# Performance work log

Measured on AMD Instinct MI355X. Metric: run time of the kernel, lower is better.

## Reference

```python
import jax, jax.numpy as jnp
import numpy as np

NUM_GRAPHS = 512


def setup_inputs() -> dict:
    key = jax.random.key(0)
    ks = jax.random.split(key, 12)
    N, E, D, H, C = 100000, 1600000, 128, 128, 10
    x = jax.random.normal(ks[0], (N, D), dtype=jnp.float32)
    edge_index = jax.random.randint(ks[1], (2, E), 0, N, dtype=jnp.int64)
    batch = jnp.sort(jax.random.randint(ks[2], (N,), 0, NUM_GRAPHS, dtype=jnp.int64))
    def glorot(k, fan_in, fan_out):
        s = jnp.sqrt(6.0 / (fan_in + fan_out))
        return jax.random.uniform(k, (fan_in, fan_out), jnp.float32, -s, s)
    return {
        "x": x, "edge_index": edge_index, "batch": batch,
        "W_init": glorot(ks[3], D, H), "b_init": jnp.zeros((H,), jnp.float32),
        "W_h0": glorot(ks[4], H, H), "b_h0": jnp.zeros((H,), jnp.float32),
        "W_h1": glorot(ks[5], H, H), "b_h1": jnp.zeros((H,), jnp.float32),
        "W_out": glorot(ks[6], H, C), "b_out": jnp.zeros((C,), jnp.float32),
    }


def reference(x, edge_index, batch, W_init, b_init, W_h0, b_h0, W_h1, b_h1, W_out, b_out):
    N = x.shape[0]
    loop = jnp.arange(N, dtype=edge_index.dtype)
    # add self-loops (PyG GCNConv default)
    row = jnp.concatenate([edge_index[0], loop])  # source
    col = jnp.concatenate([edge_index[1], loop])  # target
    # symmetric normalization D^-1/2 (A+I) D^-1/2, degrees on target index
    deg = jax.ops.segment_sum(jnp.ones_like(col, dtype=x.dtype), col, num_segments=N)
    dis = jnp.where(deg > 0, jax.lax.rsqrt(jnp.maximum(deg, 1e-12)), 0.0)
    norm = dis[row] * dis[col]  # [E+N]

    def gcn_conv(h, W, b):
        h = h @ W                                    # linear first (as in PyG)
        msg = h[row] * norm[:, None]                 # gather + scale
        return jax.ops.segment_sum(msg, col, num_segments=N) + b  # scatter-add

    h = jax.nn.relu(gcn_conv(x, W_init, b_init))
    h = jax.nn.relu(gcn_conv(h, W_h0, b_h0))
    h = jax.nn.relu(gcn_conv(h, W_h1, b_h1))
    h = gcn_conv(h, W_out, b_out)
    # global mean pooling over graphs
    sums = jax.ops.segment_sum(h, batch, num_segments=NUM_GRAPHS)
    cnt = jax.ops.segment_sum(jnp.ones((N, 1), h.dtype), batch, num_segments=NUM_GRAPHS)
    return sums / jnp.maximum(cnt, 1.0)
```

## Files before the change

### kernel.cpp

```cpp
#include <hip/hip_runtime.h>


#define SCAN_BLOCKS 64
#define SCAN_THREADS (SCAN_BLOCKS * 256)
#define SHARD_SHIFT 12

typedef unsigned short u16;
typedef unsigned int   u32;
typedef __attribute__((ext_vector_type(8))) short bf16x8;
typedef __attribute__((ext_vector_type(4))) float f32x4;

static __device__ __forceinline__ u16 f2bf(float x) {
    u32 u = __float_as_uint(x);
    u32 r = (u + 0x7fffu + ((u >> 16) & 1u)) >> 16;
    return (u16)r;
}
static __device__ __forceinline__ float bf_lo(u32 p) { return __uint_as_float(p << 16); }
static __device__ __forceinline__ float bf_hi(u32 p) { return __uint_as_float(p & 0xffff0000u); }

__global__ __launch_bounds__(256) void k_count(const int* __restrict__ col,
                                               const int* __restrict__ row,
                                               int E,
                                               int* __restrict__ cnt32, int SH,
                                               u16* __restrict__ rank) {
    int e = blockIdx.x * 256 + threadIdx.x;
    if (e < E) {
        int c = col[e];
        int s = row[e] >> SHARD_SHIFT;
        rank[e] = (u16)atomicAdd(&cnt32[c * SH + s], 1);
    }
}

__global__ __launch_bounds__(256) void k_scan1(const int* __restrict__ cnt32, int SH,
                                               int* __restrict__ tsum, int N) {
    int t = blockIdx.x * 256 + threadIdx.x;
    int strip = (N + SCAN_THREADS - 1) / SCAN_THREADS;
    int s0 = t * strip;
    int s1 = s0 + strip; if (s1 > N) s1 = N;
    int s = 0;
    for (int i = s0; i < s1; ++i) {
        int tot = 0;
        for (int q = 0; q < SH; ++q) tot += cnt32[i * SH + q];
        s += (tot + 3) & ~3;
    }
    tsum[t] = s;
}

__global__ __launch_bounds__(1024) void k_scan2(int* __restrict__ tsum) {
    __shared__ int part[1024];
    int t = threadIdx.x;
    int base = t * 16;
    int local[16];
    int s = 0;
    #pragma unroll
    for (int i = 0; i < 16; ++i) { local[i] = tsum[base + i]; s += local[i]; }
    part[t] = s;
    __syncthreads();
    for (int off = 1; off < 1024; off <<= 1) {
        int v = part[t];
        int add = (t >= off) ? part[t - off] : 0;
        __syncthreads();
        part[t] = v + add;
        __syncthreads();
    }
    int run = (t == 0) ? 0 : part[t - 1];
    #pragma unroll
    for (int i = 0; i < 16; ++i) { int c = local[i]; tsum[base + i] = run; run += c; }
}

__global__ __launch_bounds__(256) void k_scan3(const int* __restrict__ cnt32, int SH,
                                               const int* __restrict__ tsum,
                                               int* __restrict__ rowptr,
                                               int* __restrict__ segbase,
                                               float* __restrict__ dis,
                                               int* __restrict__ csr, int N) {
    int t = blockIdx.x * 256 + threadIdx.x;
    int strip = (N + SCAN_THREADS - 1) / SCAN_THREADS;
    int s0 = t * strip;
    int s1 = s0 + strip; if (s1 > N) s1 = N;
    int run = tsum[t];
    for (int i = s0; i < s1; ++i) {
        rowptr[i] = run;
        int acc = 0;
        for (int q = 0; q < SH; ++q) {
            segbase[i * SH + q] = run + acc;
            acc += cnt32[i * SH + q];
        }
        int c = acc;
        int r = (c + 3) & ~3;
        for (int p = run + c; p < run + r; ++p) csr[p] = N;
        run += r;
        dis[i] = rsqrtf((float)(c + 1));
    }
    if (t == SCAN_THREADS - 1) rowptr[N] = run;
}

__global__ __launch_bounds__(256) void k_fill(const int* __restrict__ row,
                                              const int* __restrict__ col, int E,
                                              const int* __restrict__ segbase, int SH,
                                              const u16* __restrict__ rank,
                                              int* __restrict__ csr) {
    int e = blockIdx.x * 256 + threadIdx.x;
    if (e < E) {
        int c = col[e];
        int src = row[e];
        int s = src >> SHARD_SHIFT;
        csr[segbase[c * SH + s] + (int)rank[e]] = src;
    }
}

__global__ __launch_bounds__(256) void k_cast(const float* __restrict__ src,
                                              const float* __restrict__ dis,
                                              u16* __restrict__ bX,
                                              u16* __restrict__ bA,
                                              u16* __restrict__ bB, int N) {
    int i = blockIdx.x * 256 + threadIdx.x;
    int total = (N + 1) * 32;
    if (i >= total) return;
    int v = i >> 5;
    if (v < N) {
        float dv = dis[v];
        float4 val = ((const float4*)src)[i];
        ushort4 o;
        o.x = f2bf(dv * val.x); o.y = f2bf(dv * val.y);
        o.z = f2bf(dv * val.z); o.w = f2bf(dv * val.w);
        ((ushort4*)bX)[i] = o;
    } else {
        ushort4 z = {0, 0, 0, 0};
        ((ushort4*)bX)[i] = z;
        ((ushort4*)bA)[i] = z;
        ((ushort4*)bB)[i] = z;
    }
}

__global__ __launch_bounds__(256) void k_wprep4(const float* __restrict__ W0,
                                                const float* __restrict__ W1,
                                                const float* __restrict__ W2,
                                                const float* __restrict__ Wo,
                                                u32* __restrict__ whi,
                                                u32* __restrict__ wlo, int C) {
    if (blockIdx.x < 24) {
        int which = blockIdx.x >> 3;
        const float* W = (which == 0) ? W0 : (which == 1) ? W1 : W2;
        int t = (blockIdx.x & 7) * 256 + threadIdx.x;
        int lane = t & 63;
        int nk = t >> 6;
        int k0 = nk & 3;
        int ntile = nk >> 2;
        int n = ntile * 16 + (lane & 15);
        int kbase = k0 * 32 + (lane >> 4) * 8;
        u32 hi[4], lo[4];
        #pragma unroll
        for (int tt = 0; tt < 4; ++tt) {
            float w0 = W[(kbase + 2 * tt) * 128 + n];
            float w1 = W[(kbase + 2 * tt + 1) * 128 + n];
            u16 h0 = f2bf(w0), h1 = f2bf(w1);
            u16 l0 = f2bf(w0 - __uint_as_float((u32)h0 << 16));
            u16 l1 = f2bf(w1 - __uint_as_float((u32)h1 << 16));
            hi[tt] = (u32)h0 | ((u32)h1 << 16);
            lo[tt] = (u32)l0 | ((u32)l1 << 16);
        }
        uint4 qh = {hi[0], hi[1], hi[2], hi[3]};
        uint4 ql = {lo[0], lo[1], lo[2], lo[3]};
        int base = which * 2048;
        ((uint4*)whi)[base + t] = qh;
        ((uint4*)wlo)[base + t] = ql;
    } else {
        int t = threadIdx.x;
        int lane = t & 63;
        int k0 = t >> 6;
        int n = lane & 15;
        int kbase = k0 * 32 + (lane >> 4) * 8;
        bool vc = (n < C);
        u32 hi[4], lo[4];
        #pragma unroll
        for (int tt = 0; tt < 4; ++tt) {
            float w0 = vc ? Wo[(kbase + 2 * tt) * C + n] : 0.f;
            float w1 = vc ? Wo[(kbase + 2 * tt + 1) * C + n] : 0.f;
            u16 h0 = f2bf(w0), h1 = f2bf(w1);
            u16 l0 = f2bf(w0 - __uint_as_float((u32)h0 << 16));
            u16 l1 = f2bf(w1 - __uint_as_float((u32)h1 << 16));
            hi[tt] = (u32)h0 | ((u32)h1 << 16);
            lo[tt] = (u32)l0 | ((u32)l1 << 16);
        }
        uint4 qh = {hi[0], hi[1], hi[2], hi[3]};
        uint4 ql = {lo[0], lo[1], lo[2], lo[3]};
        ((uint4*)whi)[6144 + t] = qh;
        ((uint4*)wlo)[6144 + t] = ql;
    }
}

__global__ __launch_bounds__(256) void k_fused(const u16* __restrict__ hin,
                                               const u32* __restrict__ whi,
                                               const u32* __restrict__ wlo,
                                               const float* __restrict__ bias,
                                               u16* __restrict__ hout,
                                               const int* __restrict__ rowptr,
                                               const int* __restrict__ csr,
                                               const float* __restrict__ dis,
                                               int N, int scale_out,
                                               int proj,
                                               const u32* __restrict__ pwhi,
                                               const u32* __restrict__ pwlo,
                                               float* __restrict__ tmpC) {
    __shared__ u32 sS[32 * 68];
    __shared__ float dS[32];
    int tid = threadIdx.x;
    int wave = tid >> 6;
    int lane = tid & 63;
    int row0 = blockIdx.x * 32;
    const uint4* hin4 = (const uint4*)hin;

    int grp = lane >> 4;
    int sub = lane & 15;
    #pragma unroll
    for (int jj = 0; jj < 2; ++jj) {
        int rloc = wave * 8 + jj * 4 + grp;
        int row = row0 + rloc;
        bool hR = row < N;
        int ia = 0, rem = 0;
        float dv = 1.f;
        if (hR) {
            ia  = rowptr[row];
            rem = rowptr[row + 1] - ia;
            dv  = dis[row];
        }
        int nself = hR ? row : N;
        uint4 ps = hin4[((u32)nself << 4) + sub];
        float a0 = bf_lo(ps.x), a1 = bf_hi(ps.x);
        float a2 = bf_lo(ps.y), a3 = bf_hi(ps.y);
        float a4 = bf_lo(ps.z), a5 = bf_hi(ps.z);
        float a6 = bf_lo(ps.w), a7 = bf_hi(ps.w);
        int m = rem;
        m = max(m, __shfl_xor(m, 16));
        m = max(m, __shfl_xor(m, 32));
        const int4* cq = (const int4*)(csr + ia);
        for (int k = 0; k < m; k += 8) {
            int4 q0 = cq[(k >> 2)];
            int4 q1 = cq[(k >> 2) + 1];
            bool v0 = k < rem;
            bool v1 = (k + 4) < rem;
            int n0 = v0 ? q0.x : N;
            int n1 = v0 ? q0.y : N;
            int n2 = v0 ? q0.z : N;
            int n3 = v0 ? q0.w : N;
            int n4 = v1 ? q1.x : N;
            int n5 = v1 ? q1.y : N;
            int n6 = v1 ? q1.z : N;
            int n7 = v1 ? q1.w : N;
            uint4 p0 = hin4[((u32)n0 << 4) + sub];
            uint4 p1 = hin4[((u32)n1 << 4) + sub];
            uint4 p2 = hin4[((u32)n2 << 4) + sub];
            uint4 p3 = hin4[((u32)n3 << 4) + sub];
            uint4 p4 = hin4[((u32)n4 << 4) + sub];
            uint4 p5 = hin4[((u32)n5 << 4) + sub];
            uint4 p6 = hin4[((u32)n6 << 4) + sub];
            uint4 p7 = hin4[((u32)n7 << 4) + sub];
            a0 += bf_lo(p0.x) + bf_lo(p1.x) + bf_lo(p2.x) + bf_lo(p3.x);
            a1 += bf_hi(p0.x) + bf_hi(p1.x) + bf_hi(p2.x) + bf_hi(p3.x);
            a2 += bf_lo(p0.y) + bf_lo(p1.y) + bf_lo(p2.y) + bf_lo(p3.y);
            a3 += bf_hi(p0.y) + bf_hi(p1.y) + bf_hi(p2.y) + bf_hi(p3.y);
            a4 += bf_lo(p0.z) + bf_lo(p1.z) + bf_lo(p2.z) + bf_lo(p3.z);
            a5 += bf_hi(p0.z) + bf_hi(p1.z) + bf_hi(p2.z) + bf_hi(p3.z);
            a6 += bf_lo(p0.w) + bf_lo(p1.w) + bf_lo(p2.w) + bf_lo(p3.w);
            a7 += bf_hi(p0.w) + bf_hi(p1.w) + bf_hi(p2.w) + bf_hi(p3.w);
            a0 += bf_lo(p4.x) + bf_lo(p5.x) + bf_lo(p6.x) + bf_lo(p7.x);
            a1 += bf_hi(p4.x) + bf_hi(p5.x) + bf_hi(p6.x) + bf_hi(p7.x);
            a2 += bf_lo(p4.y) + bf_lo(p5.y) + bf_lo(p6.y) + bf_lo(p7.y);
            a3 += bf_hi(p4.y) + bf_hi(p5.y) + bf_hi(p6.y) + bf_hi(p7.y);
            a4 += bf_lo(p4.z) + bf_lo(p5.z) + bf_lo(p6.z) + bf_lo(p7.z);
            a5 += bf_hi(p4.z) + bf_hi(p5.z) + bf_hi(p6.z) + bf_hi(p7.z);
            a6 += bf_lo(p4.w) + bf_lo(p5.w) + bf_lo(p6.w) + bf_lo(p7.w);
            a7 += bf_hi(p4.w) + bf_hi(p5.w) + bf_hi(p6.w) + bf_hi(p7.w);
        }
        u32 w0 = (u32)f2bf(dv * a0) | ((u32)f2bf(dv * a1) << 16);
        u32 w1 = (u32)f2bf(dv * a2) | ((u32)f2bf(dv * a3) << 16);
        u32 w2 = (u32)f2bf(dv * a4) | ((u32)f2bf(dv * a5) << 16);
        u32 w3 = (u32)f2bf(dv * a6) | ((u32)f2bf(dv * a7) << 16);
        sS[rloc * 65 + sub * 4 + 0] = w0;
        sS[rloc * 65 + sub * 4 + 1] = w1;
        sS[rloc * 65 + sub * 4 + 2] = w2;
        sS[rloc * 65 + sub * 4 + 3] = w3;
        if (sub == 0) dS[rloc] = dv;
    }
    __syncthreads();

    f32x4 acc[2][2] = {{{0.f,0.f,0.f,0.f},{0.f,0.f,0.f,0.f}},
                       {{0.f,0.f,0.f,0.f},{0.f,0.f,0.f,0.f}}};
    int mA = lane & 15;
    int qA = lane >> 4;
    #pragma unroll
    for (int k0 = 0; k0 < 4; ++k0) {
        union { u32 u[4]; bf16x8 v; } A0, A1;
        int ub = k0 * 16 + qA * 4;
        #pragma unroll
        for (int tt = 0; tt < 4; ++tt) {
            A0.u[tt] = sS[mA * 65 + ub + tt];
            A1.u[tt] = sS[(mA + 16) * 65 + ub + tt];
        }
        #pragma unroll
        for (int ct = 0; ct < 2; ++ct) {
            int ntk = ((2 * wave + ct) * 4 + k0) * 64 + lane;
            union { uint4 q; bf16x8 v; } BH, BL;
            BH.q = ((const uint4*)whi)[ntk];
            BL.q = ((const uint4*)wlo)[ntk];
            acc[0][ct] = __builtin_amdgcn_mfma_f32_16x16x32_bf16(A0.v, BH.v, acc[0][ct], 0, 0, 0);
            acc[0][ct] = __builtin_amdgcn_mfma_f32_16x16x32_bf16(A0.v, BL.v, acc[0][ct], 0, 0, 0);
            acc[1][ct] = __builtin_amdgcn_mfma_f32_16x16x32_bf16(A1.v, BH.v, acc[1][ct], 0, 0, 0);
            acc[1][ct] = __builtin_amdgcn_mfma_f32_16x16x32_bf16(A1.v, BL.v, acc[1][ct], 0, 0, 0);
        }
    }

    if (!proj) {
        #pragma unroll
        for (int rt = 0; rt < 2; ++rt) {
            #pragma unroll
            for (int ct = 0; ct < 2; ++ct) {
                int col = (2 * wave + ct) * 16 + (lane & 15);
                float bb = bias[col];
                #pragma unroll
                for (int r = 0; r < 4; ++r) {
                    int rloc = rt * 16 + (lane >> 4) * 4 + r;
                    int row = row0 + rloc;
                    if (row < N) {
                        float o = fmaxf(acc[rt][ct][r] + bb, 0.f);
                        if (scale_out) o *= dS[rloc];
                        hout[((u32)row << 7) + col] = f2bf(o);
                    }
                }
            }
        }
    } else {
        __syncthreads();
        u16* hS16 = (u16*)sS;
        #pragma unroll
        for (int rt = 0; rt < 2; ++rt) {
            #pragma unroll
            for (int ct = 0; ct < 2; ++ct) {
                int col = (2 * wave + ct) * 16 + (lane & 15);
                float bb = bias[col];
                #pragma unroll
                for (int r = 0; r < 4; ++r) {
                    int rloc = rt * 16 + (lane >> 4) * 4 + r;
                    hS16[rloc * 136 + col] = f2bf(fmaxf(acc[rt][ct][r] + bb, 0.f));
                }
            }
        }
        __syncthreads();
        if (wave < 2) {
            int m2 = lane & 15;
            int quad = lane >> 4;
            f32x4 a2 = {0.f, 0.f, 0.f, 0.f};
            #pragma unroll
            for (int k0 = 0; k0 < 4; ++k0) {
                bf16x8 Afrag = *(bf16x8*)&hS16[(wave * 16 + m2) * 136 + k0 * 32 + quad * 8];
                union { uint4 q; bf16x8 v; } BH, BL;
                BH.q = ((const uint4*)pwhi)[k0 * 64 + lane];
                BL.q = ((const uint4*)pwlo)[k0 * 64 + lane];
                a2 = __builtin_amdgcn_mfma_f32_16x16x32_bf16(Afrag, BH.v, a2, 0, 0, 0);
                a2 = __builtin_amdgcn_mfma_f32_16x16x32_bf16(Afrag, BL.v, a2, 0, 0, 0);
            }
            #pragma unroll
            for (int r = 0; r < 4; ++r) {
                int rloc = wave * 16 + quad * 4 + r;
                int row = row0 + rloc;
                if (row < N) tmpC[((u32)row << 4) + m2] = a2[r] * dS[rloc];
            }
        }
        if (blockIdx.x == 0 && tid < 16) tmpC[((u32)N << 4) + tid] = 0.f;
    }
}

__global__ __launch_bounds__(1024) void k_aggpool(const float* __restrict__ tp,
                                                  const int* __restrict__ rowptr,
                                                  const int* __restrict__ csr,
                                                  const float* __restrict__ dis,
                                                  const int* __restrict__ batch,
                                                  const float* __restrict__ bout,
                                                  float* __restrict__ out,
                                                  int N, int C) {
    __shared__ float red[1024];
    int g = blockIdx.x;
    int tid = threadIdx.x;
    int c = tid & 15;
    int rg = tid >> 4;
    int lo = 0, hi = N;
    while (lo < hi) { int m = (lo + hi) >> 1; if (batch[m] < g) lo = m + 1; else hi = m; }
    int lb = lo;
    hi = N;
    while (lo < hi) { int m = (lo + hi) >> 1; if (batch[m] <= g) lo = m + 1; else hi = m; }
    int ub = lo;
    const int4* csr4 = (const int4*)csr;
    float pacc = 0.f;
    for (int v = lb + rg; v < ub; v += 64) {
        float acc = tp[((u32)v << 4) + c];
        int i = rowptr[v], e = rowptr[v + 1];
        for (; i + 8 <= e; i += 8) {
            int4 q0 = csr4[(u32)i >> 2];
            int4 q1 = csr4[((u32)i >> 2) + 1];
            acc += tp[((u32)q0.x << 4) + c] + tp[((u32)q0.y << 4) + c]
                 + tp[((u32)q0.z << 4) + c] + tp[((u32)q0.w << 4) + c]
                 + tp[((u32)q1.x << 4) + c] + tp[((u32)q1.y << 4) + c]
                 + tp[((u32)q1.z << 4) + c] + tp[((u32)q1.w << 4) + c];
        }
        if (i < e) {
            int4 q0 = csr4[(u32)i >> 2];
            acc += tp[((u32)q0.x << 4) + c] + tp[((u32)q0.y << 4) + c]
                 + tp[((u32)q0.z << 4) + c] + tp[((u32)q0.w << 4) + c];
        }
        pacc += dis[v] * acc;
    }
    red[tid] = pacc;
    __syncthreads();
    #pragma unroll
    for (int s = 32; s >= 1; s >>= 1) {
        if (rg < s) red[tid] += red[tid + s * 16];
        __syncthreads();
    }
    if (tid < C) {
        float cnt = (float)(ub - lb);
        out[g * C + tid] = (red[tid] + cnt * bout[tid]) / fmaxf(cnt, 1.0f);
    }
}

extern "C" void kernel_launch(void* const* d_in, const int* in_sizes, int n_in,
                              void* d_out, int out_size, void* d_ws, size_t ws_size,
                              hipStream_t stream) {
    const float* x      = (const float*)d_in[0];
    const int*   ei     = (const int*)d_in[1];
    const int*   batch  = (const int*)d_in[2];
    const float* W_init = (const float*)d_in[3];
    const float* b_init = (const float*)d_in[4];
    const float* W_h0   = (const float*)d_in[5];
    const float* b_h0   = (const float*)d_in[6];
    const float* W_h1   = (const float*)d_in[7];
    const float* b_h1   = (const float*)d_in[8];
    const float* W_out  = (const float*)d_in[9];
    const float* b_out  = (const float*)d_in[10];

    int N = in_sizes[0] / 128;
    int E = in_sizes[1] / 2;
    int C = in_sizes[10];
    int G = out_size / C;
    int SH = (N >> SHARD_SHIFT) + 1;

    size_t off = 0;
    auto alloc = [&](size_t bytes) -> char* {
        char* p = (char*)d_ws + off;
        off += (bytes + 255) & ~(size_t)255;
        return p;
    };
    u16*   bufX   = (u16*)  alloc((size_t)(N + 1) * 128 * 2);
    u16*   bufA   = (u16*)  alloc((size_t)(N + 1) * 128 * 2);
    u16*   bufB   = (u16*)  alloc((size_t)(N + 1) * 128 * 2);
    float* dis    = (float*)alloc((size_t)N * 4);
    int*   rowptr = (int*)  alloc((size_t)(N + 1) * 4);
    int*   csr    = (int*)  alloc(((size_t)E + 3 * (size_t)N + 8) * 4);
    int*   tsum   = (int*)  alloc((size_t)SCAN_THREADS * 4);
    u32*   whi    = (u32*)  alloc((3 * 2048 + 256) * 16);
    u32*   wlo    = (u32*)  alloc((3 * 2048 + 256) * 16);
    int*   segbase= (int*)  alloc((size_t)N * SH * 4);
    size_t zoff   = off;
    int*   cnt32  = (int*)  alloc((size_t)N * SH * 4);
    size_t zbytes = off - zoff;

    u16*   rank   = (u16*)bufB;
    float* tmpC   = (float*)bufX;

    hipMemsetAsync(cnt32, 0, zbytes, stream);

    const int* rowi = ei;
    const int* coli = ei + E;

    int eb = (E + 255) / 256;
    k_count<<<eb, 256, 0, stream>>>(coli, rowi, E, cnt32, SH, rank);
    k_scan1<<<SCAN_BLOCKS, 256, 0, stream>>>(cnt32, SH, tsum, N);
    k_scan2<<<1, 1024, 0, stream>>>(tsum);
    k_scan3<<<SCAN_BLOCKS, 256, 0, stream>>>(cnt32, SH, tsum, rowptr, segbase, dis, csr, N);
    k_fill<<<eb, 256, 0, stream>>>(rowi, coli, E, segbase, SH, rank, csr);

    k_wprep4<<<25, 256, 0, stream>>>(W_init, W_h0, W_h1, W_out, whi, wlo, C);

    int cg = ((N + 1) * 32 + 255) / 256;
    k_cast<<<cg, 256, 0, stream>>>(x, dis, bufX, bufA, bufB, N);

    int fb = (N + 31) / 32;

    k_fused<<<fb, 256, 0, stream>>>(bufX, whi,         wlo,         b_init, bufA, rowptr, csr, dis, N, 1, 0, nullptr, nullptr, nullptr);
    k_fused<<<fb, 256, 0, stream>>>(bufA, whi + 8192,  wlo + 8192,  b_h0,   bufB, rowptr, csr, dis, N, 1, 0, nullptr, nullptr, nullptr);
    k_fused<<<fb, 256, 0, stream>>>(bufB, whi + 16384, wlo + 16384, b_h1,   bufA, rowptr, csr, dis, N, 0, 1, whi + 24576, wlo + 24576, tmpC);

    k_aggpool<<<G, 1024, 0, stream>>>(tmpC, rowptr, csr, dis, batch, b_out, (float*)d_out, N, C);
}
```

Measured before the change: 544.4 us.

## Transpose shard-count layout and split CSR scan into coalesced per-node kernels

Changes the per-(node,shard) count and segbase arrays from node-major to shard-major so that per-node kernels read them with coalesced accesses. Degree totals and the dis computation move into a new per-node kernel, so the strided scan kernels only sum a compact padded-degree array. Segment bases and padding fill move into a separate fully parallel per-node kernel. This adds two kernel launches and an extra pdeg buffer in exchange for far less serialized, strided work in the scan phase.

New measurement: 477.9 us. 1.14x faster.

```diff
diff --git a/kernel.cpp b/kernel.cpp
--- a/kernel.cpp
+++ b/kernel.cpp
@@ -21,28 +21,36 @@
 __global__ __launch_bounds__(256) void k_count(const int* __restrict__ col,
                                                const int* __restrict__ row,
                                                int E,
-                                               int* __restrict__ cnt32, int SH,
+                                               int* __restrict__ cnt32, int N,
                                                u16* __restrict__ rank) {
     int e = blockIdx.x * 256 + threadIdx.x;
     if (e < E) {
         int c = col[e];
         int s = row[e] >> SHARD_SHIFT;
-        rank[e] = (u16)atomicAdd(&cnt32[c * SH + s], 1);
-    }
-}
-
-__global__ __launch_bounds__(256) void k_scan1(const int* __restrict__ cnt32, int SH,
+        rank[e] = (u16)atomicAdd(&cnt32[s * N + c], 1);
+    }
+}
+
+__global__ __launch_bounds__(256) void k_deg(const int* __restrict__ cnt32,
+                                             int N, int SH,
+                                             int* __restrict__ pdeg,
+                                             float* __restrict__ dis) {
+    int i = blockIdx.x * 256 + threadIdx.x;
+    if (i >= N) return;
+    int tot = 0;
+    for (int q = 0; q < SH; ++q) tot += cnt32[q * N + i];
+    pdeg[i] = (tot + 3) & ~3;
+    dis[i] = rsqrtf((float)(tot + 1));
+}
+
+__global__ __launch_bounds__(256) void k_scan1(const int* __restrict__ pdeg,
                                                int* __restrict__ tsum, int N) {
     int t = blockIdx.x * 256 + threadIdx.x;
     int strip = (N + SCAN_THREADS - 1) / SCAN_THREADS;
     int s0 = t * strip;
     int s1 = s0 + strip; if (s1 > N) s1 = N;
     int s = 0;
-    for (int i = s0; i < s1; ++i) {
-        int tot = 0;
-        for (int q = 0; q < SH; ++q) tot += cnt32[i * SH + q];
-        s += (tot + 3) & ~3;
-    }
+    for (int i = s0; i < s1; ++i) s += pdeg[i];
     tsum[t] = s;
 }
 
@@ -68,12 +76,9 @@
     for (int i = 0; i < 16; ++i) { int c = local[i]; tsum[base + i] = run; run += c; }
 }
 
-__global__ __launch_bounds__(256) void k_scan3(const int* __restrict__ cnt32, int SH,
+__global__ __launch_bounds__(256) void k_scan3(const int* __restrict__ pdeg,
                                                const int* __restrict__ tsum,
-                                               int* __restrict__ rowptr,
-                                               int* __restrict__ segbase,
-                                               float* __restrict__ dis,
-                                               int* __restrict__ csr, int N) {
+                                               int* __restrict__ rowptr, int N) {
     int t = blockIdx.x * 256 + threadIdx.x;
     int strip = (N + SCAN_THREADS - 1) / SCAN_THREADS;
     int s0 = t * strip;
@@ -81,23 +86,31 @@
     int run = tsum[t];
     for (int i = s0; i < s1; ++i) {
         rowptr[i] = run;
-        int acc = 0;
-        for (int q = 0; q < SH; ++q) {
-            segbase[i * SH + q] = run + acc;
-            acc += cnt32[i * SH + q];
-        }
-        int c = acc;
-        int r = (c + 3) & ~3;
-        for (int p = run + c; p < run + r; ++p) csr[p] = N;
-        run += r;
-        dis[i] = rsqrtf((float)(c + 1));
+        run += pdeg[i];
     }
     if (t == SCAN_THREADS - 1) rowptr[N] = run;
+}
+
+__global__ __launch_bounds__(256) void k_segbase(const int* __restrict__ cnt32,
+                                                 const int* __restrict__ rowptr,
+                                                 int N, int SH,
+                                                 int* __restrict__ segbase,
+                                                 int* __restrict__ csr) {
+    int i = blockIdx.x * 256 + threadIdx.x;
+    if (i >= N) return;
+    int rp = rowptr[i];
+    int acc = 0;
+    for (int q = 0; q < SH; ++q) {
+        segbase[q * N + i] = rp + acc;
+        acc += cnt32[q * N + i];
+    }
+    int r = (acc + 3) & ~3;
+    for (int p = rp + acc; p < rp + r; ++p) csr[p] = N;
 }
 
 __global__ __launch_bounds__(256) void k_fill(const int* __restrict__ row,
                                               const int* __restrict__ col, int E,
-                                              const int* __restrict__ segbase, int SH,
+                                              const int* __restrict__ segbase, int N,
                                               const u16* __restrict__ rank,
                                               int* __restrict__ csr) {
     int e = blockIdx.x * 256 + threadIdx.x;
@@ -105,7 +118,7 @@
         int c = col[e];
         int src = row[e];
         int s = src >> SHARD_SHIFT;
-        csr[segbase[c * SH + s] + (int)rank[e]] = src;
+        csr[segbase[s * N + c] + (int)rank[e]] = src;
     }
 }
 
@@ -457,6 +470,7 @@
     int*   rowptr = (int*)  alloc((size_t)(N + 1) * 4);
     int*   csr    = (int*)  alloc(((size_t)E + 3 * (size_t)N + 8) * 4);
     int*   tsum   = (int*)  alloc((size_t)SCAN_THREADS * 4);
+    int*   pdeg   = (int*)  alloc((size_t)N * 4);
     u32*   whi    = (u32*)  alloc((3 * 2048 + 256) * 16);
     u32*   wlo    = (u32*)  alloc((3 * 2048 + 256) * 16);
     int*   segbase= (int*)  alloc((size_t)N * SH * 4);
@@ -473,11 +487,14 @@
     const int* coli = ei + E;
 
     int eb = (E + 255) / 256;
-    k_count<<<eb, 256, 0, stream>>>(coli, rowi, E, cnt32, SH, rank);
-    k_scan1<<<SCAN_BLOCKS, 256, 0, stream>>>(cnt32, SH, tsum, N);
+    int nb = (N + 255) / 256;
+    k_count<<<eb, 256, 0, stream>>>(coli, rowi, E, cnt32, N, rank);
+    k_deg<<<nb, 256, 0, stream>>>(cnt32, N, SH, pdeg, dis);
+    k_scan1<<<SCAN_BLOCKS, 256, 0, stream>>>(pdeg, tsum, N);
     k_scan2<<<1, 1024, 0, stream>>>(tsum);
-    k_scan3<<<SCAN_BLOCKS, 256, 0, stream>>>(cnt32, SH, tsum, rowptr, segbase, dis, csr, N);
-    k_fill<<<eb, 256, 0, stream>>>(rowi, coli, E, segbase, SH, rank, csr);
+    k_scan3<<<SCAN_BLOCKS, 256, 0, stream>>>(pdeg, tsum, rowptr, N);
+    k_segbase<<<nb, 256, 0, stream>>>(cnt32, rowptr, N, SH, segbase, csr);
+    k_fill<<<eb, 256, 0, stream>>>(rowi, coli, E, segbase, N, rank, csr);
 
     k_wprep4<<<25, 256, 0, stream>>>(W_init, W_h0, W_h1, W_out, whi, wlo, C);
 
```
